# Kernel optimization log

Hardware: AMD Instinct MI355X
Metric: run time of the kernel (lower is better)

The kernel has to match this reference:

```python
import jax, jax.numpy as jnp
import numpy as np

HW = 16          # feature map side before crop
P = HW * HW      # 256 spatial positions
G = 128          # output genetic channels per branch
CROP = 14        # crop size


def feature_genetic(x, idx, oh, ow):
    # x: [B, C, 16, 16]; idx: [G, P] channel index per (group, position);
    # oh, ow: [G] crop offsets in {0,1}
    B = x.shape[0]
    feat = x.reshape(B, x.shape[1], P)                 # [B, C, 256]
    pos = jnp.arange(P)
    picked = feat[:, idx, pos]                         # [B, G, 256]
    grid = picked.reshape(B, G, HW, HW)                # [B, 128, 16, 16]
    ch = jnp.arange(G)
    hidx = oh[:, None] + jnp.arange(CROP)[None, :]     # [G, 14]
    widx = ow[:, None] + jnp.arange(CROP)[None, :]     # [G, 14]
    # fancy-index crop: [B, 128, 14, 14]
    return grid[:, ch[:, None, None], hidx[:, :, None], widx[:, None, :]]


def setup_inputs() -> dict:
    key = jax.random.key(0)
    k1, k3, k5, kw, ki, kh, kw2 = jax.random.split(key, 7)
    B, C = 128, 512
    x1 = jax.random.normal(k1, (B, C, HW, HW), dtype=jnp.float32)
    x3 = jax.random.normal(k3, (B, C, HW, HW), dtype=jnp.float32)
    x5 = jax.random.normal(k5, (B, C, HW, HW), dtype=jnp.float32)
    W = jax.random.normal(kw, (768, 384), dtype=jnp.float32) * 0.02  # 1x1 conv weight
    idx = jax.random.randint(ki, (3, G, P), 0, C, dtype=jnp.int32)
    offh = jax.random.randint(kh, (3, G), 0, 2, dtype=jnp.int32)
    offw = jax.random.randint(kw2, (3, G), 0, 2, dtype=jnp.int32)
    return {"x1": x1, "x3": x3, "x5": x5, "W": W, "idx": idx, "offh": offh, "offw": offw}


def reference(x1, x3, x5, W, idx, offh, offw):
    g1 = feature_genetic(x1, idx[0], offh[0], offw[0])   # [B, 128, 14, 14]
    g3 = feature_genetic(x3, idx[1], offh[1], offw[1])
    g5 = feature_genetic(x5, idx[2], offh[2], offw[2])
    feats = jnp.concatenate((g1, g3, g5), axis=1)        # [B, 384, 14, 14]
    # 1x1 conv (no bias): Conv2d(384, 768, kernel_size=1)
    out = jnp.einsum('bchw,oc->bohw', feats, W)          # [B, 768, 14, 14]
    return out
```

## Files before the change

kernel.cpp:

```cpp
#include <hip/hip_runtime.h>
#include <hip/hip_bf16.h>

#define PIX 256
#define CROP 14
#define HW2 196
#define BB 128
#define CC 512
#define NC 384
#define NO 768
#define CAP 128

typedef __bf16 bf16x8 __attribute__((ext_vector_type(8)));
typedef __bf16 bf16x4 __attribute__((ext_vector_type(4)));
typedef float  f32x4  __attribute__((ext_vector_type(4)));
typedef unsigned int u32;

#define GLOAD_LDS16(src, dst) \
    __builtin_amdgcn_global_load_lds((const __attribute__((address_space(1))) void*)(src), \
                                     (__attribute__((address_space(3))) void*)(dst), 16, 0, 0)

__global__ void wconv_kernel(const float* __restrict__ W, __bf16* __restrict__ Wb,
                             int* __restrict__ cnt) {
    int tid = blockIdx.x * 256 + threadIdx.x;
    Wb[tid] = (__bf16)W[tid];
    if (tid < 1536) cnt[tid] = 0;
}

__global__ void fill_kernel(const int* __restrict__ idx, const int* __restrict__ offh,
                            const int* __restrict__ offw, int* __restrict__ cnt,
                            u32* __restrict__ bucket) {
    int tid = blockIdx.x * 256 + threadIdx.x;
    int c3 = tid / HW2;
    int hw = tid - c3 * HW2;
    int i = hw / CROP, j = hw - i * CROP;
    int p = (offh[c3] + i) * 16 + offw[c3] + j;
    int ch = idx[c3 * PIX + p];
    int bkt = (c3 >> 7) * 512 + ch;
    int pos = atomicAdd(&cnt[bkt], 1);
    if (pos < CAP)
        bucket[bkt * CAP + pos] =
            ((u32)(c3 & 127) << 25) | ((u32)hw << 17) | ((u32)p << 9) | (u32)ch;
}

__global__ __launch_bounds__(256) void scan_kernel(const int* __restrict__ cnt,
                                                   int* __restrict__ pref) {
    __shared__ int part[256];
    int tid = threadIdx.x;
    int loc[6];
    int s = 0;
#pragma unroll
    for (int i = 0; i < 6; ++i) {
        int v = cnt[tid * 6 + i]; if (v > CAP) v = CAP;
        loc[i] = s; s += v;
    }
    part[tid] = s;
    __syncthreads();
    if (tid < 64) {
        int l4[4]; int s4 = 0;
#pragma unroll
        for (int i = 0; i < 4; ++i) { l4[i] = s4; s4 += part[tid * 4 + i]; }
        int v = s4;
#pragma unroll
        for (int d = 1; d < 64; d <<= 1) { int u = __shfl_up(v, d); if (tid >= d) v += u; }
        int excl = v - s4;
#pragma unroll
        for (int i = 0; i < 4; ++i) part[tid * 4 + i] = excl + l4[i];
    }
    __syncthreads();
    int off = part[tid];
#pragma unroll
    for (int i = 0; i < 6; ++i) pref[tid * 6 + i] = off + loc[i];
}

__global__ __launch_bounds__(128) void compact_kernel(const int* __restrict__ cnt,
                                                      const int* __restrict__ pref,
                                                      const u32* __restrict__ bucket,
                                                      u32* __restrict__ ent) {
    int bkt = blockIdx.x;
    int E = cnt[bkt]; if (E > CAP) E = CAP;
    int tid = threadIdx.x;
    if (tid < E) ent[pref[bkt] + tid] = bucket[bkt * CAP + tid];
}

__global__ __launch_bounds__(512) void scatter_kernel(
        const float* __restrict__ x1, const float* __restrict__ x3,
        const float* __restrict__ x5, const u32* __restrict__ ent,
        const int* __restrict__ pref, __bf16* __restrict__ feats) {
    __shared__ __bf16 fl[HW2 * 128];
    __shared__ __bf16 stg[32 * 256];
    int d = blockIdx.x;
    int wg = (d & 7) * 48 + (d >> 3);
    int b = wg / 3, t = wg % 3;
    const float* x = (t == 0) ? x1 : (t == 1) ? x3 : x5;
    const float* xb = x + (size_t)b * CC * PIX;
    int tid = threadIdx.x;

    for (int ck = 0; ck < 16; ++ck) {
#pragma unroll
        for (int i = 0; i < 4; ++i) {
            int fo = i * 2048 + tid * 4;
            f32x4 v = *(const f32x4*)(xb + ck * 8192 + fo);
            bf16x4 q;
            q[0] = (__bf16)v[0]; q[1] = (__bf16)v[1];
            q[2] = (__bf16)v[2]; q[3] = (__bf16)v[3];
            *(bf16x4*)&stg[fo] = q;
        }
        __syncthreads();
        int pi = t * 512 + ck * 32;
        int e0 = pref[pi];
        int e1 = (pi + 32 >= 1536) ? 75264 : pref[pi + 32];
        for (int g = e0 + tid; g < e1; g += 512) {
            u32 wd = ent[g];
            int ch = wd & 511;
            int p  = (wd >> 9) & 255;
            int hw = (wd >> 17) & 255;
            int c3 = wd >> 25;
            fl[hw * 128 + c3] = stg[(ch & 31) * 256 + p];
        }
        __syncthreads();
    }

    const size_t obase = (size_t)b * HW2 * NC + (size_t)t * 128;
    for (int i2 = tid; i2 < HW2 * 16; i2 += 512) {
        int hw = i2 >> 4, ckk = (i2 & 15) * 8;
        *(bf16x8*)(feats + obase + (size_t)hw * NC + ckk) = *(const bf16x8*)&fl[hw * 128 + ckk];
    }
}

__global__ __launch_bounds__(256) void gemm_kernel(const __bf16* __restrict__ feats,
                                                   const __bf16* __restrict__ Wb,
                                                   float* __restrict__ out) {
    __shared__ __bf16 ldsbuf[16384];
    __bf16* Abuf = ldsbuf;
    __bf16* Bbuf = ldsbuf + 8192;

    const int d = blockIdx.x;
    const int wg = (d & 7) * 147 + (d >> 3);
    const int o_base = (wg % 6) * 128;
    const int m_base = (wg / 6) * 128;

    const int tid = threadIdx.x;
    const int wave = tid >> 6, lane = tid & 63;
    const int wo = wave >> 1, wm = wave & 1;
    const int l15 = lane & 15, g = lane >> 4;
    const int xr = l15 & 7;

    f32x4 acc[4][4] = {};

    for (int kt = 0; kt < 6; ++kt) {
        const int k0g = kt * 64;
#pragma unroll
        for (int it = 0; it < 4; ++it) {
            int ck = tid + it * 256;
            int row = ck >> 3, cc = ck & 7;
            int koff = k0g + ((cc ^ (row & 7)) << 3);
            GLOAD_LDS16(Wb    + (size_t)(o_base + row) * NC + koff, Abuf + ck * 8);
            GLOAD_LDS16(feats + (size_t)(m_base + row) * NC + koff, Bbuf + ck * 8);
        }
        __syncthreads();
#pragma unroll
        for (int k0 = 0; k0 < 64; k0 += 32) {
            const int cb = (k0 >> 3) + g;
            bf16x8 a[4], b[4];
#pragma unroll
            for (int s = 0; s < 4; ++s) {
                int arow = wo * 64 + s * 16 + l15;
                a[s] = *(const bf16x8*)&Abuf[arow * 64 + ((cb ^ xr) << 3)];
                int brow = wm * 64 + s * 16 + l15;
                b[s] = *(const bf16x8*)&Bbuf[brow * 64 + ((cb ^ xr) << 3)];
            }
#pragma unroll
            for (int os = 0; os < 4; ++os)
#pragma unroll
                for (int ms = 0; ms < 4; ++ms)
                    acc[os][ms] = __builtin_amdgcn_mfma_f32_16x16x32_bf16(a[os], b[ms], acc[os][ms], 0, 0, 0);
        }
        __syncthreads();
    }

#pragma unroll
    for (int os = 0; os < 4; ++os)
#pragma unroll
        for (int ms = 0; ms < 4; ++ms) {
            int m = m_base + wm * 64 + ms * 16 + l15;
            int bb = m / HW2;
            int hw = m - bb * HW2;
            int o = o_base + wo * 64 + os * 16 + g * 4;
            float* dst = out + ((size_t)bb * NO + o) * HW2 + hw;
            f32x4 v = acc[os][ms];
            dst[0 * HW2] = v[0];
            dst[1 * HW2] = v[1];
            dst[2 * HW2] = v[2];
            dst[3 * HW2] = v[3];
        }
}

extern "C" void kernel_launch(void* const* d_in, const int* in_sizes, int n_in,
                              void* d_out, int out_size, void* d_ws, size_t ws_size,
                              hipStream_t stream) {
    const float* x1   = (const float*)d_in[0];
    const float* x3   = (const float*)d_in[1];
    const float* x5   = (const float*)d_in[2];
    const float* W    = (const float*)d_in[3];
    const int*   idx  = (const int*)d_in[4];
    const int*   offh = (const int*)d_in[5];
    const int*   offw = (const int*)d_in[6];
    float* out = (float*)d_out;

    char* ws = (char*)d_ws;
    __bf16* feats  = (__bf16*)(ws);
    __bf16* Wb     = (__bf16*)(ws + 19267584);
    int*    cnt    = (int*)   (ws + 19857408);
    int*    pref   = (int*)   (ws + 19863552);
    u32*    bucket = (u32*)   (ws + 19869696);
    u32*    ent    = (u32*)   (ws + 20656128);

    wconv_kernel<<<(NO * NC) / 256, 256, 0, stream>>>(W, Wb, cnt);
    fill_kernel<<<(NC * HW2) / 256, 256, 0, stream>>>(idx, offh, offw, cnt, bucket);
    scan_kernel<<<1, 256, 0, stream>>>(cnt, pref);
    compact_kernel<<<1536, 128, 0, stream>>>(cnt, pref, bucket, ent);
    scatter_kernel<<<384, 512, 0, stream>>>(x1, x3, x5, ent, pref, feats);
    gemm_kernel<<<1176, 256, 0, stream>>>(feats, Wb, out);
}
```

Measured before the change: 110.9 us.

## Software-pipeline scatter kernel with double-buffered 16-channel staging and register prefetch

The scatter kernel now loads the next 16-channel slice of the input and its gather entries into registers while the current slice is being scattered from LDS. Staging is double-buffered across two smaller LDS buffers, and the chunk boundaries come from a small shared table. The goal is to hide global-load latency in this memory-bound kernel, which runs with few blocks per CU. The cost is twice as many chunks and barriers, more registers, and an assumption that each 16-channel chunk has at most 2048 entries.

```diff
diff --git a/kernel.cpp b/kernel.cpp
--- a/kernel.cpp
+++ b/kernel.cpp
@@ -87,7 +87,8 @@
         const float* __restrict__ x5, const u32* __restrict__ ent,
         const int* __restrict__ pref, __bf16* __restrict__ feats) {
     __shared__ __bf16 fl[HW2 * 128];
-    __shared__ __bf16 stg[32 * 256];
+    __shared__ __bf16 stg[2][16 * 256];
+    __shared__ int eb[33];
     int d = blockIdx.x;
     int wg = (d & 7) * 48 + (d >> 3);
     int b = wg / 3, t = wg % 3;
@@ -95,27 +96,64 @@
     const float* xb = x + (size_t)b * CC * PIX;
     int tid = threadIdx.x;
 
-    for (int ck = 0; ck < 16; ++ck) {
-#pragma unroll
-        for (int i = 0; i < 4; ++i) {
-            int fo = i * 2048 + tid * 4;
-            f32x4 v = *(const f32x4*)(xb + ck * 8192 + fo);
-            bf16x4 q;
-            q[0] = (__bf16)v[0]; q[1] = (__bf16)v[1];
-            q[2] = (__bf16)v[2]; q[3] = (__bf16)v[3];
-            *(bf16x4*)&stg[fo] = q;
-        }
-        __syncthreads();
-        int pi = t * 512 + ck * 32;
-        int e0 = pref[pi];
-        int e1 = (pi + 32 >= 1536) ? 75264 : pref[pi + 32];
-        for (int g = e0 + tid; g < e1; g += 512) {
-            u32 wd = ent[g];
-            int ch = wd & 511;
-            int p  = (wd >> 9) & 255;
-            int hw = (wd >> 17) & 255;
-            int c3 = wd >> 25;
-            fl[hw * 128 + c3] = stg[(ch & 31) * 256 + p];
+    if (tid < 33) eb[tid] = (t == 2 && tid == 32) ? 75264 : pref[t * 512 + tid * 16];
+    f32x4 va = *(const f32x4*)(xb + tid * 4);
+    f32x4 vb = *(const f32x4*)(xb + 2048 + tid * 4);
+    __syncthreads();
+
+    u32 wd[4];
+    {
+        int e0 = eb[0], e1 = eb[1];
+#pragma unroll
+        for (int k = 0; k < 4; ++k) {
+            int g = e0 + tid + k * 512;
+            wd[k] = (g < e1) ? ent[g] : 0xFFFFFFFFu;
+        }
+        bf16x4 qa, qb;
+        qa[0] = (__bf16)va[0]; qa[1] = (__bf16)va[1]; qa[2] = (__bf16)va[2]; qa[3] = (__bf16)va[3];
+        qb[0] = (__bf16)vb[0]; qb[1] = (__bf16)vb[1]; qb[2] = (__bf16)vb[2]; qb[3] = (__bf16)vb[3];
+        *(bf16x4*)&stg[0][tid * 4] = qa;
+        *(bf16x4*)&stg[0][2048 + tid * 4] = qb;
+    }
+    __syncthreads();
+
+    int cur = 0;
+    for (int ck = 0; ck < 32; ++ck) {
+        f32x4 na, nb;
+        u32 wdn[4];
+        if (ck < 31) {
+            const float* nx = xb + (ck + 1) * 4096;
+            na = *(const f32x4*)(nx + tid * 4);
+            nb = *(const f32x4*)(nx + 2048 + tid * 4);
+            int ne0 = eb[ck + 1], ne1 = eb[ck + 2];
+#pragma unroll
+            for (int k = 0; k < 4; ++k) {
+                int g = ne0 + tid + k * 512;
+                wdn[k] = (g < ne1) ? ent[g] : 0xFFFFFFFFu;
+            }
+        }
+#pragma unroll
+        for (int k = 0; k < 4; ++k) {
+            u32 w = wd[k];
+            if (w != 0xFFFFFFFFu) {
+                int ch = w & 511;
+                int p  = (w >> 9) & 255;
+                int hw = (w >> 17) & 255;
+                int c3 = (int)(w >> 25);
+                fl[hw * 128 + c3] = stg[cur][(ch & 15) * 256 + p];
+            }
+        }
+        __syncthreads();
+        if (ck < 31) {
+            __bf16* s = stg[cur ^ 1];
+            bf16x4 qa, qb;
+            qa[0] = (__bf16)na[0]; qa[1] = (__bf16)na[1]; qa[2] = (__bf16)na[2]; qa[3] = (__bf16)na[3];
+            qb[0] = (__bf16)nb[0]; qb[1] = (__bf16)nb[1]; qb[2] = (__bf16)nb[2]; qb[3] = (__bf16)nb[3];
+            *(bf16x4*)&s[tid * 4] = qa;
+            *(bf16x4*)&s[2048 + tid * 4] = qb;
+#pragma unroll
+            for (int k = 0; k < 4; ++k) wd[k] = wdn[k];
+            cur ^= 1;
         }
         __syncthreads();
     }
```

Result: faster. 102.3 us (-7.7%).
